# Kernel optimization log

Measured on AMD Instinct MI355X. Metric: run time of the kernel, lower is better.

Reference implementation:

```python
import jax, jax.numpy as jnp
import numpy as np

N = 50000      # nodes
E = 800000     # edges (before self loops)
IN = 256       # in_dim
HID = 32       # hidden_dim per head
H = 8          # heads layer 1
OUT = 64       # out_dim (classes)
NEG_SLOPE = 0.2  # PyG GATConv default


def gat_conv(x, ei, W, a_src, a_dst, b, heads, ch, concat):
    """PyG GATConv (eval mode, self-loops already in ei).
    x: [n, f_in], ei: [2, e] (row0=src j, row1=dst i), W: [f_in, heads*ch],
    a_src/a_dst: [heads, ch], b: [heads*ch] or [ch]."""
    n = x.shape[0]
    h = (x @ W).reshape(n, heads, ch)                      # [n, H, C]
    src, dst = ei[0], ei[1]
    alpha_src = (h * a_src).sum(-1)                        # [n, H]
    alpha_dst = (h * a_dst).sum(-1)                        # [n, H]
    e = jax.nn.leaky_relu(alpha_src[src] + alpha_dst[dst], NEG_SLOPE)  # [e, H]
    # segment softmax over incoming edges of each dst node
    emax = jax.lax.stop_gradient(jax.ops.segment_max(e, dst, num_segments=n))
    p = jnp.exp(e - emax[dst])
    denom = jax.ops.segment_sum(p, dst, num_segments=n)    # [n, H] (>0: self loops)
    alpha = p / denom[dst]                                 # [e, H]
    out = jax.ops.segment_sum(h[src] * alpha[:, :, None], dst, num_segments=n)  # [n, H, C]
    out = out.reshape(n, heads * ch) if concat else out.mean(axis=1)
    return out + b


def setup_inputs() -> dict:
    key = jax.random.key(0)
    ks = jax.random.split(key, 9)
    x = jax.random.normal(ks[0], (N, IN), jnp.float32)
    edge_index = jax.random.randint(ks[1], (2, E), 0, N, jnp.int32)
    W1 = jax.random.normal(ks[2], (IN, H * HID), jnp.float32) * 0.05
    a_src1 = jax.random.normal(ks[3], (H, HID), jnp.float32) * 0.1
    a_dst1 = jax.random.normal(ks[4], (H, HID), jnp.float32) * 0.1
    b1 = jnp.zeros((H * HID,), jnp.float32)
    W2 = jax.random.normal(ks[5], (H * HID, OUT), jnp.float32) * 0.05
    a_src2 = jax.random.normal(ks[6], (1, OUT), jnp.float32) * 0.1
    a_dst2 = jax.random.normal(ks[7], (1, OUT), jnp.float32) * 0.1
    b2 = jnp.zeros((OUT,), jnp.float32)
    return {"x": x, "edge_index": edge_index, "W1": W1, "a_src1": a_src1,
            "a_dst1": a_dst1, "b1": b1, "W2": W2, "a_src2": a_src2,
            "a_dst2": a_dst2, "b2": b2}


def reference(x, edge_index, W1, a_src1, a_dst1, b1, W2, a_src2, a_dst2, b2):
    n = x.shape[0]
    loops = jnp.arange(n, dtype=edge_index.dtype)
    ei = jnp.concatenate([edge_index, jnp.stack([loops, loops])], axis=1)  # add self loops
    h = gat_conv(x, ei, W1, a_src1, a_dst1, b1, H, HID, concat=True)
    h = jax.nn.relu(h)
    h = gat_conv(h, ei, W2, a_src2, a_dst2, b2, 1, OUT, concat=False)
    return jax.nn.log_softmax(h, axis=1)
```

## Files before the change

### kernel.cpp

```cpp
#include <hip/hip_runtime.h>
#include <math.h>

#define NNODES 50000
#define EORIG  800000
#define ETOT   850000
#define NBUCK  196
#define BSTRIDE 5120
#define P2CHUNK 4096
#define NBLK2  ((ETOT + P2CHUNK - 1)/P2CHUNK)

typedef __attribute__((ext_vector_type(8))) short bf8_t;
typedef __attribute__((ext_vector_type(4))) float f4_t;
typedef __attribute__((ext_vector_type(2))) float f2_t;

constexpr float LOG2E = 1.44269504f;

constexpr size_t align256(size_t x){ return (x + 255) & ~size_t(255); }
constexpr size_t OFF_OFFSETS = 0;
constexpr size_t OFF_DEG     = OFF_OFFSETS + align256((size_t)NNODES*4);
constexpr size_t OFF_GCUR    = OFF_DEG     + align256((size_t)NNODES*4);
constexpr size_t OFF_EPACK   = OFF_GCUR    + align256(NBUCK*4);
constexpr size_t OFF_SRC     = OFF_EPACK   + align256((size_t)NBUCK*BSTRIDE*4);
constexpr size_t OFF_AS1     = OFF_SRC     + align256((size_t)NBUCK*BSTRIDE*4);
constexpr size_t OFF_AD1     = OFF_AS1     + align256((size_t)NNODES*8*4);
constexpr size_t OFF_W1T     = OFF_AD1     + align256((size_t)NNODES*8*4);
constexpr size_t OFF_W2T     = OFF_W1T     + align256(256*256*2);
constexpr size_t OFF_H1F8    = OFF_W2T     + align256(64*256*2);
constexpr size_t OFF_OUT1B   = OFF_H1F8    + align256((size_t)NNODES*256);
constexpr size_t OFF_H2B     = OFF_H1F8;
constexpr size_t OFF_AS2     = OFF_OUT1B   + align256((size_t)NNODES*256*2);
constexpr size_t OFF_AD2     = OFF_AS2     + align256((size_t)NNODES*4);

__device__ __forceinline__ unsigned short f2bf(float f){
    union { float f; unsigned u; } v; v.f = f;
    unsigned r = v.u + 0x7FFF + ((v.u >> 16) & 1);
    return (unsigned short)(r >> 16);
}
__device__ __forceinline__ float bf2f(unsigned short s){
    union { unsigned u; float f; } v; v.u = ((unsigned)s) << 16;
    return v.f;
}


__global__ __launch_bounds__(256) void ginit(int* __restrict__ gcur){
    int t = threadIdx.x;
    if (t < NBUCK) gcur[t] = t * BSTRIDE;
}

__global__ __launch_bounds__(256) void p3_part(const int* __restrict__ ei, int* __restrict__ gcur,
                                               int* __restrict__ epack){
    __shared__ int h[NBUCK];
    __shared__ int r[NBUCK];
    const int t = threadIdx.x;
    for (int i = t; i < NBUCK; i += 256){ h[i] = 0; r[i] = 0; }
    __syncthreads();
    const int base = blockIdx.x * P2CHUNK;
    int srcs[P2CHUNK/256], dsts[P2CHUNK/256];
#pragma unroll
    for (int j = 0; j < P2CHUNK/256; j++){
        int e = base + j*256 + t;
        if (e < ETOT){
            if (e < EORIG){ srcs[j] = ei[e]; dsts[j] = ei[EORIG + e]; }
            else          { srcs[j] = dsts[j] = e - EORIG; }
            atomicAdd(&h[dsts[j] >> 8], 1);
        } else dsts[j] = -1;
    }
    __syncthreads();
    for (int i = t; i < NBUCK; i += 256){
        int c = h[i];
        h[i] = c ? atomicAdd(&gcur[i], c) : 0;
    }
    __syncthreads();
#pragma unroll
    for (int j = 0; j < P2CHUNK/256; j++){
        if (dsts[j] >= 0){
            int b = dsts[j] >> 8;
            int rk = atomicAdd(&r[b], 1);
            epack[h[b] + rk] = (srcs[j] << 8) | (dsts[j] & 255);
        }
    }
}

__global__ __launch_bounds__(256) void p4_csr(const int* __restrict__ gcur, const int* __restrict__ epack,
                                              int* __restrict__ offsets, int* __restrict__ deg_g,
                                              int* __restrict__ srclist){
    __shared__ int deg[256];
    __shared__ int sm[256];
    __shared__ int cur[256];
    const int b = blockIdx.x, t = threadIdx.x;
    const int s0 = b * BSTRIDE, s1 = gcur[b];
    deg[t] = 0; __syncthreads();
    for (int i = s0 + t; i < s1; i += 256) atomicAdd(&deg[epack[i] & 255], 1);
    __syncthreads();
    int v = deg[t];
    sm[t] = v; __syncthreads();
    for (int off = 1; off < 256; off <<= 1){
        int add = (t >= off) ? sm[t-off] : 0;
        __syncthreads();
        sm[t] += add;
        __syncthreads();
    }
    int excl = sm[t] - v;
    int node = (b << 8) + t;
    if (node < NNODES){ offsets[node] = s0 + excl; deg_g[node] = v; }
    cur[t] = s0 + excl;
    __syncthreads();
    for (int i = s0 + t; i < s1; i += 256){
        int p = epack[i];
        int pos = atomicAdd(&cur[p & 255], 1);
        srclist[pos] = p >> 8;
    }
}


__global__ __launch_bounds__(256) void conv_w_k(const float* __restrict__ W1, const float* __restrict__ W2,
                                                short* __restrict__ w1t, short* __restrict__ w2t){
    int o = blockIdx.x*256 + threadIdx.x;
    if (o < 256*256){
        int n = o >> 8, k = o & 255;
        w1t[o] = (short)f2bf(W1[k*256 + n]);
    } else {
        int o2 = o - 256*256;
        if (o2 < 64*256){
            int n = o2 >> 8, k = o2 & 255;
            w2t[o2] = (short)f2bf(W2[k*64 + n]);
        }
    }
}


__global__ __launch_bounds__(512) void gemm1_mfma(const float* __restrict__ x, const short* __restrict__ w1t,
        const float* __restrict__ a1s, const float* __restrict__ a1d,
        unsigned char* __restrict__ h1f8, float* __restrict__ as1, float* __restrict__ ad1){
    __shared__ short As[128][40];
    __shared__ short Bs[256][40];
    const int t = threadIdx.x;
    const int lane = t & 63, wave = t >> 6;
    const int wy = wave >> 2, wx = wave & 3;
    const int quad = lane >> 4, l15 = lane & 15;
    const int r0 = blockIdx.x * 128;
    const int srow = t >> 2, skoff = (t & 3) * 8;
    f4_t zero4 = {0.f,0.f,0.f,0.f};
    f4_t acc[4][4];
#pragma unroll
    for (int i=0;i<4;i++)
#pragma unroll
      for (int j=0;j<4;j++) acc[i][j] = zero4;

    for (int kk = 0; kk < 256; kk += 32){
        float4 xa0 = {0,0,0,0}, xa1 = {0,0,0,0};
        if (r0 + srow < NNODES){
            xa0 = *(const float4*)(x + (size_t)(r0+srow)*256 + kk + skoff);
            xa1 = *(const float4*)(x + (size_t)(r0+srow)*256 + kk + skoff + 4);
        }
        bf8_t b0  = *(const bf8_t*)(w1t + (size_t)(srow      )*256 + kk + skoff);
        bf8_t b1v = *(const bf8_t*)(w1t + (size_t)(srow + 128)*256 + kk + skoff);
        bf8_t a0;
        a0[0]=f2bf(xa0.x); a0[1]=f2bf(xa0.y); a0[2]=f2bf(xa0.z); a0[3]=f2bf(xa0.w);
        a0[4]=f2bf(xa1.x); a0[5]=f2bf(xa1.y); a0[6]=f2bf(xa1.z); a0[7]=f2bf(xa1.w);
        __syncthreads();
        *(bf8_t*)&As[srow     ][skoff] = a0;
        *(bf8_t*)&Bs[srow     ][skoff] = b0;
        *(bf8_t*)&Bs[srow+128][skoff] = b1v;
        __syncthreads();
        bf8_t af[4], bfr[4];
#pragma unroll
        for (int i=0;i<4;i++) af[i]  = *(const bf8_t*)&As[wy*64 + i*16 + l15][quad*8];
#pragma unroll
        for (int j=0;j<4;j++) bfr[j] = *(const bf8_t*)&Bs[wx*64 + j*16 + l15][quad*8];
#pragma unroll
        for (int i=0;i<4;i++)
#pragma unroll
          for (int j=0;j<4;j++)
            acc[i][j] = __builtin_amdgcn_mfma_f32_16x16x32_bf16(af[i], bfr[j], acc[i][j], 0,0,0);
    }
    const int colbase = wx*64;
    const int head0 = colbase >> 5;
    float cs[4], cd[4];
#pragma unroll
    for (int j=0;j<4;j++){
        cs[j] = a1s[colbase + j*16 + l15] * LOG2E;
        cd[j] = a1d[colbase + j*16 + l15] * LOG2E;
    }
#pragma unroll
    for (int i=0;i<4;i++){
        int rowb = r0 + wy*64 + i*16 + quad*4;
#pragma unroll
        for (int reg=0; reg<4; reg++){
            int row = rowb + reg;
            bool valid = row < NNODES;
            float sp0=0.f, dp0=0.f, sp1=0.f, dp1=0.f;
#pragma unroll
            for (int j=0;j<4;j++){
                float v = acc[i][j][reg];
                if (j < 2){ sp0 += v*cs[j]; dp0 += v*cd[j]; }
                else      { sp1 += v*cs[j]; dp1 += v*cd[j]; }
                if (valid){
                    unsigned enc = (unsigned)__builtin_amdgcn_cvt_pk_fp8_f32(v, v, 0, false);
                    h1f8[(size_t)row*256 + colbase + j*16 + l15] = (unsigned char)(enc & 0xffu);
                }
            }
            sp0 += __shfl_xor(sp0,1); sp0 += __shfl_xor(sp0,2); sp0 += __shfl_xor(sp0,4); sp0 += __shfl_xor(sp0,8);
            dp0 += __shfl_xor(dp0,1); dp0 += __shfl_xor(dp0,2); dp0 += __shfl_xor(dp0,4); dp0 += __shfl_xor(dp0,8);
            sp1 += __shfl_xor(sp1,1); sp1 += __shfl_xor(sp1,2); sp1 += __shfl_xor(sp1,4); sp1 += __shfl_xor(sp1,8);
            dp1 += __shfl_xor(dp1,1); dp1 += __shfl_xor(dp1,2); dp1 += __shfl_xor(dp1,4); dp1 += __shfl_xor(dp1,8);
            if (valid && l15 == 0){
                as1[row*8 + head0    ] = sp0;
                ad1[row*8 + head0    ] = dp0;
                as1[row*8 + head0 + 1] = sp1;
                ad1[row*8 + head0 + 1] = dp1;
            }
        }
    }
}


__global__ __launch_bounds__(256) void gemm2_mfma(const short* __restrict__ ab, const short* __restrict__ w2t,
        const float* __restrict__ a2s, const float* __restrict__ a2d,
        short* __restrict__ h2b, float* __restrict__ as2, float* __restrict__ ad2){
    __shared__ short As[128][40];
    __shared__ short Bs[64][40];
    const int t = threadIdx.x;
    const int lane = t & 63, wave = t >> 6;
    const int quad = lane >> 4, l15 = lane & 15;
    const int r0 = blockIdx.x * 128;
    const int srow = t >> 2, skoff = (t & 3) * 8;
    f4_t zero4 = {0.f,0.f,0.f,0.f};
    f4_t acc[2][4];
#pragma unroll
    for (int i=0;i<2;i++)
#pragma unroll
      for (int j=0;j<4;j++) acc[i][j] = zero4;

    for (int kk = 0; kk < 256; kk += 32){
        bf8_t a0 = {}, a1v = {};
        if (r0 + srow < NNODES)      a0  = *(const bf8_t*)(ab + (size_t)(r0+srow)*256 + kk + skoff);
        if (r0 + srow + 64 < NNODES) a1v = *(const bf8_t*)(ab + (size_t)(r0+srow+64)*256 + kk + skoff);
        bf8_t b0 = *(const bf8_t*)(w2t + (size_t)srow*256 + kk + skoff);
        __syncthreads();
        *(bf8_t*)&As[srow   ][skoff] = a0;
        *(bf8_t*)&As[srow+64][skoff] = a1v;
        *(bf8_t*)&Bs[srow   ][skoff] = b0;
        __syncthreads();
        bf8_t af[2], bfr[4];
#pragma unroll
        for (int i=0;i<2;i++) af[i]  = *(const bf8_t*)&As[wave*32 + i*16 + l15][quad*8];
#pragma unroll
        for (int j=0;j<4;j++) bfr[j] = *(const bf8_t*)&Bs[j*16 + l15][quad*8];
#pragma unroll
        for (int i=0;i<2;i++)
#pragma unroll
          for (int j=0;j<4;j++)
            acc[i][j] = __builtin_amdgcn_mfma_f32_16x16x32_bf16(af[i], bfr[j], acc[i][j], 0,0,0);
    }
    float cs[4], cd[4];
#pragma unroll
    for (int j=0;j<4;j++){
        cs[j] = a2s[j*16 + l15] * LOG2E;
        cd[j] = a2d[j*16 + l15] * LOG2E;
    }
#pragma unroll
    for (int i=0;i<2;i++){
        int rowb = r0 + wave*32 + i*16 + quad*4;
#pragma unroll
        for (int reg=0; reg<4; reg++){
            int row = rowb + reg;
            bool valid = row < NNODES;
            float sp=0.f, dp=0.f;
#pragma unroll
            for (int j=0;j<4;j++){
                float v = acc[i][j][reg];
                sp += v*cs[j]; dp += v*cd[j];
                if (valid) h2b[(size_t)row*64 + j*16 + l15] = (short)f2bf(v);
            }
            sp += __shfl_xor(sp,1); sp += __shfl_xor(sp,2); sp += __shfl_xor(sp,4); sp += __shfl_xor(sp,8);
            dp += __shfl_xor(dp,1); dp += __shfl_xor(dp,2); dp += __shfl_xor(dp,4); dp += __shfl_xor(dp,8);
            if (valid && l15 == 0){ as2[row] = sp; ad2[row] = dp; }
        }
    }
}


__global__ __launch_bounds__(256) void aggregate1_k(const unsigned char* __restrict__ h1f8,
        const float* __restrict__ as1, const float* __restrict__ ad1,
        const int* __restrict__ offsets, const int* __restrict__ deg_g,
        const int* __restrict__ srclist,
        const float* __restrict__ b1, short* __restrict__ out1b){
    int d = blockIdx.x*4 + (threadIdx.x >> 6);
    int lane = threadIdx.x & 63;
    if (d >= NNODES) return;
    int hh = lane >> 3;
    int start = offsets[d];
    int end = start + deg_g[d];
    float ad_h = ad1[d*8 + hh];
    float denom = 0.f;
    f2_t acc01 = {0.f,0.f}, acc23 = {0.f,0.f};
    int k = start;
    for (; k + 3 < end; k += 4){
        int s0 = srclist[k], s1 = srclist[k+1], s2 = srclist[k+2], s3 = srclist[k+3];
        float e0 = as1[s0*8 + hh] + ad_h;
        float e1 = as1[s1*8 + hh] + ad_h;
        float e2 = as1[s2*8 + hh] + ad_h;
        float e3 = as1[s3*8 + hh] + ad_h;
        unsigned w0 = *(const unsigned*)(h1f8 + (size_t)s0*256 + lane*4);
        unsigned w1 = *(const unsigned*)(h1f8 + (size_t)s1*256 + lane*4);
        unsigned w2 = *(const unsigned*)(h1f8 + (size_t)s2*256 + lane*4);
        unsigned w3 = *(const unsigned*)(h1f8 + (size_t)s3*256 + lane*4);
        e0 = fmaxf(0.2f*e0, e0); e1 = fmaxf(0.2f*e1, e1);
        e2 = fmaxf(0.2f*e2, e2); e3 = fmaxf(0.2f*e3, e3);
        float p0 = exp2f(e0), p1 = exp2f(e1), p2 = exp2f(e2), p3 = exp2f(e3);
        denom += (p0 + p1) + (p2 + p3);
        f2_t lo0 = __builtin_amdgcn_cvt_pk_f32_fp8(w0, false), hi0 = __builtin_amdgcn_cvt_pk_f32_fp8(w0, true);
        f2_t lo1 = __builtin_amdgcn_cvt_pk_f32_fp8(w1, false), hi1 = __builtin_amdgcn_cvt_pk_f32_fp8(w1, true);
        f2_t lo2 = __builtin_amdgcn_cvt_pk_f32_fp8(w2, false), hi2 = __builtin_amdgcn_cvt_pk_f32_fp8(w2, true);
        f2_t lo3 = __builtin_amdgcn_cvt_pk_f32_fp8(w3, false), hi3 = __builtin_amdgcn_cvt_pk_f32_fp8(w3, true);
        acc01 += p0*lo0 + p1*lo1 + p2*lo2 + p3*lo3;
        acc23 += p0*hi0 + p1*hi1 + p2*hi2 + p3*hi3;
    }
    for (; k < end; k++){
        int s0 = srclist[k];
        float e0 = as1[s0*8 + hh] + ad_h;
        unsigned w0 = *(const unsigned*)(h1f8 + (size_t)s0*256 + lane*4);
        e0 = fmaxf(0.2f*e0, e0);
        float p0 = exp2f(e0);
        denom += p0;
        f2_t lo0 = __builtin_amdgcn_cvt_pk_f32_fp8(w0, false), hi0 = __builtin_amdgcn_cvt_pk_f32_fp8(w0, true);
        acc01 += p0*lo0;
        acc23 += p0*hi0;
    }
    float inv = 1.f / denom;
    float4 bv = *(const float4*)(b1 + lane*4);
    ushort4 us;
    us.x = f2bf(fmaxf(acc01[0]*inv + bv.x, 0.f));
    us.y = f2bf(fmaxf(acc01[1]*inv + bv.y, 0.f));
    us.z = f2bf(fmaxf(acc23[0]*inv + bv.z, 0.f));
    us.w = f2bf(fmaxf(acc23[1]*inv + bv.w, 0.f));
    *(ushort4*)(out1b + (size_t)d*256 + lane*4) = us;
}

__global__ __launch_bounds__(256) void aggregate2_k(const unsigned short* __restrict__ h2b,
        const float* __restrict__ as2, const float* __restrict__ ad2,
        const int* __restrict__ offsets, const int* __restrict__ deg_g,
        const int* __restrict__ srclist,
        const float* __restrict__ b2, float* __restrict__ out){
    int d = blockIdx.x*4 + (threadIdx.x >> 6);
    int lane = threadIdx.x & 63;
    if (d >= NNODES) return;
    int start = offsets[d];
    int end = start + deg_g[d];
    float ad_v = ad2[d];
    float denom = 0.f, acc = 0.f;
    int k = start;
    for (; k + 3 < end; k += 4){
        int s0 = srclist[k], s1 = srclist[k+1], s2 = srclist[k+2], s3 = srclist[k+3];
        float e0 = as2[s0] + ad_v;
        float e1 = as2[s1] + ad_v;
        float e2 = as2[s2] + ad_v;
        float e3 = as2[s3] + ad_v;
        unsigned short u0 = h2b[(size_t)s0*64 + lane];
        unsigned short u1 = h2b[(size_t)s1*64 + lane];
        unsigned short u2 = h2b[(size_t)s2*64 + lane];
        unsigned short u3 = h2b[(size_t)s3*64 + lane];
        e0 = fmaxf(0.2f*e0, e0); e1 = fmaxf(0.2f*e1, e1);
        e2 = fmaxf(0.2f*e2, e2); e3 = fmaxf(0.2f*e3, e3);
        float p0 = exp2f(e0), p1 = exp2f(e1), p2 = exp2f(e2), p3 = exp2f(e3);
        denom += (p0 + p1) + (p2 + p3);
        acc += p0*bf2f(u0) + p1*bf2f(u1) + p2*bf2f(u2) + p3*bf2f(u3);
    }
    for (; k < end; k++){
        int s0 = srclist[k];
        float e0 = as2[s0] + ad_v;
        unsigned short u0 = h2b[(size_t)s0*64 + lane];
        e0 = fmaxf(0.2f*e0, e0);
        float p0 = exp2f(e0);
        denom += p0;
        acc += p0*bf2f(u0);
    }
    float v = acc/denom + b2[lane];
    float mx = v;
#pragma unroll
    for (int off = 1; off < 64; off <<= 1) mx = fmaxf(mx, __shfl_xor(mx, off));
    float ex = __expf(v - mx);
    float ss = ex;
#pragma unroll
    for (int off = 1; off < 64; off <<= 1) ss += __shfl_xor(ss, off);
    out[(size_t)d*64 + lane] = v - mx - __logf(ss);
}


extern "C" void kernel_launch(void* const* d_in, const int* in_sizes, int n_in,
                              void* d_out, int out_size, void* d_ws, size_t ws_size,
                              hipStream_t stream){
    const float* x      = (const float*)d_in[0];
    const int*   ei     = (const int*)  d_in[1];
    const float* W1     = (const float*)d_in[2];
    const float* a_src1 = (const float*)d_in[3];
    const float* a_dst1 = (const float*)d_in[4];
    const float* b1     = (const float*)d_in[5];
    const float* W2     = (const float*)d_in[6];
    const float* a_src2 = (const float*)d_in[7];
    const float* a_dst2 = (const float*)d_in[8];
    const float* b2     = (const float*)d_in[9];

    char* ws = (char*)d_ws;
    int*   offsets = (int*)  (ws + OFF_OFFSETS);
    int*   deg_g   = (int*)  (ws + OFF_DEG);
    int*   gcur    = (int*)  (ws + OFF_GCUR);
    int*   epack   = (int*)  (ws + OFF_EPACK);
    int*   srclist = (int*)  (ws + OFF_SRC);
    float* as1     = (float*)(ws + OFF_AS1);
    float* ad1     = (float*)(ws + OFF_AD1);
    short* w1t     = (short*)(ws + OFF_W1T);
    short* w2t     = (short*)(ws + OFF_W2T);
    unsigned char* h1f8 = (unsigned char*)(ws + OFF_H1F8);
    short* out1b   = (short*)(ws + OFF_OUT1B);
    short* h2b     = (short*)(ws + OFF_H2B);
    float* as2     = (float*)(ws + OFF_AS2);
    float* ad2     = (float*)(ws + OFF_AD2);

    ginit  <<<1, 256, 0, stream>>>(gcur);
    p3_part<<<NBLK2, 256, 0, stream>>>(ei, gcur, epack);
    p4_csr <<<NBUCK, 256, 0, stream>>>(gcur, epack, offsets, deg_g, srclist);

    conv_w_k<<<(256*256 + 64*256 + 255)/256, 256, 0, stream>>>(W1, W2, w1t, w2t);

    gemm1_mfma<<<(NNODES+127)/128, 512, 0, stream>>>(x, w1t, a_src1, a_dst1, h1f8, as1, ad1);
    aggregate1_k<<<(NNODES+3)/4, 256, 0, stream>>>(h1f8, as1, ad1, offsets, deg_g, srclist, b1, out1b);

    gemm2_mfma<<<(NNODES+127)/128, 256, 0, stream>>>(out1b, w2t, a_src2, a_dst2, h2b, as2, ad2);
    aggregate2_k<<<(NNODES+3)/4, 256, 0, stream>>>((const unsigned short*)h2b, as2, ad2, offsets, deg_g, srclist, b2, (float*)d_out);
}
```

Baseline: 262.5 us.

## Compute edge weights cooperatively across lanes and broadcast via shuffles in aggregation

Both aggregation kernels now load up to 64 source indices per wave at once. Each lane computes attention weights for a distinct (edge, head) pair, and the weights and indices are broadcast with shuffles, so lanes no longer redundantly gather as1/as2 and repeat the exp per edge. The gcur init moves into the weight-conversion kernel, which removes one launch. This adds shuffle overhead and padding for low-degree nodes, which average about 17 edges.

```diff
diff --git a/kernel.cpp b/kernel.cpp
--- a/kernel.cpp
+++ b/kernel.cpp
@@ -42,11 +42,6 @@
 }
 
 
-__global__ __launch_bounds__(256) void ginit(int* __restrict__ gcur){
-    int t = threadIdx.x;
-    if (t < NBUCK) gcur[t] = t * BSTRIDE;
-}
-
 __global__ __launch_bounds__(256) void p3_part(const int* __restrict__ ei, int* __restrict__ gcur,
                                                int* __restrict__ epack){
     __shared__ int h[NBUCK];
@@ -114,8 +109,10 @@
 
 
 __global__ __launch_bounds__(256) void conv_w_k(const float* __restrict__ W1, const float* __restrict__ W2,
-                                                short* __restrict__ w1t, short* __restrict__ w2t){
+                                                short* __restrict__ w1t, short* __restrict__ w2t,
+                                                int* __restrict__ gcur){
     int o = blockIdx.x*256 + threadIdx.x;
+    if (o < NBUCK) gcur[o] = o * BSTRIDE;
     if (o < 256*256){
         int n = o >> 8, k = o & 255;
         w1t[o] = (short)f2bf(W1[k*256 + n]);
@@ -289,44 +286,42 @@
     int d = blockIdx.x*4 + (threadIdx.x >> 6);
     int lane = threadIdx.x & 63;
     if (d >= NNODES) return;
-    int hh = lane >> 3;
+    const int head_g = lane >> 3;
+    const int head_p = lane & 7;
+    const int ep     = lane >> 3;
     int start = offsets[d];
-    int end = start + deg_g[d];
-    float ad_h = ad1[d*8 + hh];
+    int deg = deg_g[d];
+    float ad_p = ad1[d*8 + head_p];
     float denom = 0.f;
     f2_t acc01 = {0.f,0.f}, acc23 = {0.f,0.f};
-    int k = start;
-    for (; k + 3 < end; k += 4){
-        int s0 = srclist[k], s1 = srclist[k+1], s2 = srclist[k+2], s3 = srclist[k+3];
-        float e0 = as1[s0*8 + hh] + ad_h;
-        float e1 = as1[s1*8 + hh] + ad_h;
-        float e2 = as1[s2*8 + hh] + ad_h;
-        float e3 = as1[s3*8 + hh] + ad_h;
-        unsigned w0 = *(const unsigned*)(h1f8 + (size_t)s0*256 + lane*4);
-        unsigned w1 = *(const unsigned*)(h1f8 + (size_t)s1*256 + lane*4);
-        unsigned w2 = *(const unsigned*)(h1f8 + (size_t)s2*256 + lane*4);
-        unsigned w3 = *(const unsigned*)(h1f8 + (size_t)s3*256 + lane*4);
-        e0 = fmaxf(0.2f*e0, e0); e1 = fmaxf(0.2f*e1, e1);
-        e2 = fmaxf(0.2f*e2, e2); e3 = fmaxf(0.2f*e3, e3);
-        float p0 = exp2f(e0), p1 = exp2f(e1), p2 = exp2f(e2), p3 = exp2f(e3);
-        denom += (p0 + p1) + (p2 + p3);
-        f2_t lo0 = __builtin_amdgcn_cvt_pk_f32_fp8(w0, false), hi0 = __builtin_amdgcn_cvt_pk_f32_fp8(w0, true);
-        f2_t lo1 = __builtin_amdgcn_cvt_pk_f32_fp8(w1, false), hi1 = __builtin_amdgcn_cvt_pk_f32_fp8(w1, true);
-        f2_t lo2 = __builtin_amdgcn_cvt_pk_f32_fp8(w2, false), hi2 = __builtin_amdgcn_cvt_pk_f32_fp8(w2, true);
-        f2_t lo3 = __builtin_amdgcn_cvt_pk_f32_fp8(w3, false), hi3 = __builtin_amdgcn_cvt_pk_f32_fp8(w3, true);
-        acc01 += p0*lo0 + p1*lo1 + p2*lo2 + p3*lo3;
-        acc23 += p0*hi0 + p1*hi1 + p2*hi2 + p3*hi3;
-    }
-    for (; k < end; k++){
-        int s0 = srclist[k];
-        float e0 = as1[s0*8 + hh] + ad_h;
-        unsigned w0 = *(const unsigned*)(h1f8 + (size_t)s0*256 + lane*4);
-        e0 = fmaxf(0.2f*e0, e0);
-        float p0 = exp2f(e0);
-        denom += p0;
-        f2_t lo0 = __builtin_amdgcn_cvt_pk_f32_fp8(w0, false), hi0 = __builtin_amdgcn_cvt_pk_f32_fp8(w0, true);
-        acc01 += p0*lo0;
-        acc23 += p0*hi0;
+    for (int w = 0; w < deg; w += 64){
+        int deg_w = min(64, deg - w);
+        int s_reg = srclist[start + w + min(lane, deg_w-1)];
+        int ngr = (deg_w + 7) >> 3;
+        auto comp_p = [&](int g)->float{
+            int ei = g*8 + ep;
+            int s  = __shfl(s_reg, min(ei, deg_w-1));
+            float e = as1[s*8 + head_p] + ad_p;
+            e = fmaxf(0.2f*e, e);
+            float p = exp2f(e);
+            return (ei < deg_w) ? p : 0.f;
+        };
+        float p_reg = comp_p(0);
+        for (int g = 0; g < ngr; g++){
+            float p_cur = p_reg;
+            if (g + 1 < ngr) p_reg = comp_p(g+1);
+#pragma unroll
+            for (int e = 0; e < 8; e++){
+                float pe = __shfl(p_cur, e*8 + head_g);
+                int   se = __shfl(s_reg, g*8 + e);
+                unsigned wv = *(const unsigned*)(h1f8 + (size_t)se*256 + lane*4);
+                f2_t lo = __builtin_amdgcn_cvt_pk_f32_fp8(wv, false);
+                f2_t hi = __builtin_amdgcn_cvt_pk_f32_fp8(wv, true);
+                acc01 += pe*lo;
+                acc23 += pe*hi;
+                denom += pe;
+            }
+        }
     }
     float inv = 1.f / denom;
     float4 bv = *(const float4*)(b1 + lane*4);
@@ -347,34 +342,27 @@
     int lane = threadIdx.x & 63;
     if (d >= NNODES) return;
     int start = offsets[d];
-    int end = start + deg_g[d];
+    int deg = deg_g[d];
     float ad_v = ad2[d];
     float denom = 0.f, acc = 0.f;
-    int k = start;
-    for (; k + 3 < end; k += 4){
-        int s0 = srclist[k], s1 = srclist[k+1], s2 = srclist[k+2], s3 = srclist[k+3];
-        float e0 = as2[s0] + ad_v;
-        float e1 = as2[s1] + ad_v;
-        float e2 = as2[s2] + ad_v;
-        float e3 = as2[s3] + ad_v;
-        unsigned short u0 = h2b[(size_t)s0*64 + lane];
-        unsigned short u1 = h2b[(size_t)s1*64 + lane];
-        unsigned short u2 = h2b[(size_t)s2*64 + lane];
-        unsigned short u3 = h2b[(size_t)s3*64 + lane];
-        e0 = fmaxf(0.2f*e0, e0); e1 = fmaxf(0.2f*e1, e1);
-        e2 = fmaxf(0.2f*e2, e2); e3 = fmaxf(0.2f*e3, e3);
-        float p0 = exp2f(e0), p1 = exp2f(e1), p2 = exp2f(e2), p3 = exp2f(e3);
-        denom += (p0 + p1) + (p2 + p3);
-        acc += p0*bf2f(u0) + p1*bf2f(u1) + p2*bf2f(u2) + p3*bf2f(u3);
-    }
-    for (; k < end; k++){
-        int s0 = srclist[k];
-        float e0 = as2[s0] + ad_v;
-        unsigned short u0 = h2b[(size_t)s0*64 + lane];
-        e0 = fmaxf(0.2f*e0, e0);
-        float p0 = exp2f(e0);
-        denom += p0;
-        acc += p0*bf2f(u0);
+    for (int w = 0; w < deg; w += 64){
+        int deg_w = min(64, deg - w);
+        int s_reg = srclist[start + w + min(lane, deg_w-1)];
+        float ev = as2[s_reg] + ad_v;
+        ev = fmaxf(0.2f*ev, ev);
+        float p_lane = (lane < deg_w) ? exp2f(ev) : 0.f;
+        int ngr = (deg_w + 7) >> 3;
+        for (int g = 0; g < ngr; g++){
+#pragma unroll
+            for (int e2 = 0; e2 < 8; e2++){
+                int ee = g*8 + e2;
+                float pe = __shfl(p_lane, ee);
+                int   se = __shfl(s_reg, ee);
+                float hv = bf2f(h2b[(size_t)se*64 + lane]);
+                acc += pe*hv;
+                denom += pe;
+            }
+        }
     }
     float v = acc/denom + b2[lane];
     float mx = v;
@@ -418,12 +406,11 @@
     float* as2     = (float*)(ws + OFF_AS2);
     float* ad2     = (float*)(ws + OFF_AD2);
 
-    ginit  <<<1, 256, 0, stream>>>(gcur);
+    conv_w_k<<<(256*256 + 64*256 + 255)/256, 256, 0, stream>>>(W1, W2, w1t, w2t, gcur);
+
     p3_part<<<NBLK2, 256, 0, stream>>>(ei, gcur, epack);
     p4_csr <<<NBUCK, 256, 0, stream>>>(gcur, epack, offsets, deg_g, srclist);
 
-    conv_w_k<<<(256*256 + 64*256 + 255)/256, 256, 0, stream>>>(W1, W2, w1t, w2t);
-
     gemm1_mfma<<<(NNODES+127)/128, 512, 0, stream>>>(x, w1t, a_src1, a_dst1, h1f8, as1, ad1);
     aggregate1_k<<<(NNODES+3)/4, 256, 0, stream>>>(h1f8, as1, ad1, offsets, deg_g, srclist, b1, out1b);
 
```

New measurement: 249.4 us. 5.0% less time.
